# Optimization experiments

Hardware: AMD Instinct MI355X
Metric: run time of the kernel (lower is better)

The kernel has to match this reference:

```python
import jax, jax.numpy as jnp
import numpy as np

B, S, CL = 64, 250, 16
WV, CV, FV, LAB = 50000, 100, 10, 20
WD, CD, CH, FD, HD = 300, 300, 50, 5, 200
T = LAB + 2          # CRF lattice size (labels + START + STOP)
START, STOP = LAB, LAB + 1
H = HD // 2          # hidden per LSTM direction
IN = CH + WD + FD    # 355


def _lstm_dir(x, m, w_ih, w_hh, b):
    # x: [B,S,IN], m: [B,S] bool -> masked unidirectional LSTM (PyTorch gate order i,f,g,o)
    Bn = x.shape[0]
    def step(carry, inp):
        h, c = carry
        xt, mt = inp
        g = xt @ w_ih.T + h @ w_hh.T + b
        i, f, gg, o = jnp.split(g, 4, axis=-1)
        c_new = jax.nn.sigmoid(f) * c + jax.nn.sigmoid(i) * jnp.tanh(gg)
        h_new = jax.nn.sigmoid(o) * jnp.tanh(c_new)
        mt = mt[:, None]
        h = jnp.where(mt, h_new, h)
        c = jnp.where(mt, c_new, c)
        return (h, c), h
    init = (jnp.zeros((Bn, H), x.dtype), jnp.zeros((Bn, H), x.dtype))
    _, hs = jax.lax.scan(step, init, (x.transpose(1, 0, 2), m.T))
    return hs.transpose(1, 0, 2)  # [B,S,H]


def _viterbi(feats, mask, trans):
    # feats: [B,S,T], mask: [B,S] bool, trans: [T,T] (trans[i,j] = score i->j)
    Bn = feats.shape[0]
    delta0 = trans[START][None, :] + feats[:, 0]  # [B,T]
    ident = jnp.arange(T)[None, :]
    def step(delta, inp):
        f_t, m_t = inp                              # [B,T], [B]
        sc = delta[:, :, None] + trans[None]        # [B,T(prev),T(cur)]
        vmax = sc.max(axis=1)
        bp = sc.argmax(axis=1)                      # [B,T]
        m = m_t[:, None]
        delta = jnp.where(m, vmax + f_t, delta)
        bp = jnp.where(m, bp, ident)                # pads: pass-through pointer
        return delta, bp
    delta, bps = jax.lax.scan(step, delta0,
                              (feats[:, 1:].transpose(1, 0, 2), mask[:, 1:].T))
    final = delta + trans[:, STOP][None, :]
    score = final.max(axis=1)                       # [B]
    last = final.argmax(axis=1)                     # [B]
    ar = jnp.arange(Bn)
    def back(tag, bp):
        prev = bp[ar, tag]
        return prev, prev
    _, prevs = jax.lax.scan(back, last, bps, reverse=True)  # [S-1,B]
    tag_seq = jnp.concatenate([prevs.transpose(1, 0), last[:, None]], axis=1)  # [B,S]
    return score, tag_seq


def setup_inputs() -> dict:
    key = jax.random.key(0)
    ks = jax.random.split(key, 20)
    lens = jax.random.randint(ks[0], (B,), S // 2, S + 1)
    mask = (jnp.arange(S)[None, :] < lens[:, None])
    def u(k, shape, scale):
        return jax.random.uniform(k, shape, jnp.float32, -scale, scale)
    return {
        "batch_word": jax.random.randint(ks[1], (B, S), 0, WV),
        "batch_features": jax.random.randint(ks[2], (B, S), 0, FV),
        "batch_wordlen": lens,
        "batch_char": jax.random.randint(ks[3], (B * S, CL), 0, CV),
        "batch_charlen": jax.random.randint(ks[4], (B * S,), 1, CL + 1),
        "batch_charrecover": jnp.arange(B * S),
        "mask": mask,
        "char_emb": u(ks[5], (CV, CD), np.sqrt(3.0 / CD)),
        "word_emb": u(ks[6], (WV, WD), np.sqrt(3.0 / WD)),
        "feat_emb": u(ks[7], (FV, FD), np.sqrt(3.0 / FD)),
        "conv_w": 0.1 * jax.random.normal(ks[8], (CH, CD, 3), jnp.float32),
        "conv_b": jnp.zeros((CH,), jnp.float32),
        "w_ih_f": 0.1 * jax.random.normal(ks[9], (4 * H, IN), jnp.float32),
        "w_hh_f": 0.1 * jax.random.normal(ks[10], (4 * H, H), jnp.float32),
        "b_f": jnp.zeros((4 * H,), jnp.float32),
        "w_ih_b": 0.1 * jax.random.normal(ks[11], (4 * H, IN), jnp.float32),
        "w_hh_b": 0.1 * jax.random.normal(ks[12], (4 * H, H), jnp.float32),
        "b_b": jnp.zeros((4 * H,), jnp.float32),
        "proj_w": 0.1 * jax.random.normal(ks[13], (HD, T), jnp.float32),
        "proj_b": jnp.zeros((T,), jnp.float32),
        "trans": 0.1 * jax.random.normal(ks[14], (T, T), jnp.float32),
    }


def reference(batch_word, batch_features, batch_wordlen, batch_char, batch_charlen,
              batch_charrecover, mask, char_emb, word_emb, feat_emb, conv_w, conv_b,
              w_ih_f, w_hh_f, b_f, w_ih_b, w_hh_b, b_b, proj_w, proj_b, trans):
    # char CNN: embed -> conv1d(k=3, pad=1) -> global max-pool (dropout: eval mode, identity)
    ce = char_emb[batch_char]                          # [B*S, CL, CD]
    conv = jax.lax.conv_general_dilated(
        ce.transpose(0, 2, 1), conv_w, window_strides=(1,), padding=[(1, 1)],
        dimension_numbers=('NCH', 'OIH', 'NCH')) + conv_b[None, :, None]
    char_feat = conv.max(axis=2)                       # [B*S, CH]
    char_feat = char_feat[batch_charrecover].reshape(B, S, CH)
    word_rep = jnp.concatenate(
        [word_emb[batch_word], char_feat, feat_emb[batch_features]], axis=2)  # [B,S,IN]
    # masked BiLSTM (equivalent to pack_padded_sequence: pads never update state)
    h_f = _lstm_dir(word_rep, mask, w_ih_f, w_hh_f, b_f)
    h_b = _lstm_dir(word_rep[:, ::-1], mask[:, ::-1], w_ih_b, w_hh_b, b_b)[:, ::-1]
    lstm_out = jnp.concatenate([h_f, h_b], axis=2)     # [B,S,HD]
    feats = lstm_out @ proj_w + proj_b                 # [B,S,T]
    score, tag_seq = _viterbi(feats, mask, trans)
    return tag_seq
```

## Files before the change

### kernel.cpp

```cpp
#include <hip/hip_runtime.h>
#include <hip/hip_bf16.h>
#include <math.h>

#define WS_U        0
#define WS_WPAD     15360
#define WS_WREP     359424
#define WS_PRE      6503424
#define WS_LSTM     359424
#define WS_FEATS    3559424

__global__ __launch_bounds__(256) void prepw_kernel(
    const float* __restrict__ wf, const float* __restrict__ wb,
    float* __restrict__ w_pad) {
  int idx = blockIdx.x * 256 + threadIdx.x;
  if (idx >= 896 * 384) return;
  int col = idx % 384, row = idx / 384;
  float v = 0.f;
  if (col < 355) {
    if (row < 400)      v = wf[row * 355 + col];
    else if (row < 800) v = wb[(row - 400) * 355 + col];
  }
  w_pad[idx] = v;
}

__global__ __launch_bounds__(256) void u_kernel(
    const float* __restrict__ char_emb, const float* __restrict__ conv_w,
    float* __restrict__ U) {
  int idx = blockIdx.x * 256 + threadIdx.x;
  if (idx >= 15000) return;
  int c = idx / 150, rem = idx % 150, k = rem / 50, o = rem % 50;
  float acc = 0.f;
  for (int i = 0; i < 300; i++)
    acc += char_emb[c * 300 + i] * conv_w[(o * 300 + i) * 3 + k];
  U[idx] = acc;
}

__global__ __launch_bounds__(64) void assemble_kernel(
    const int* __restrict__ batch_word, const int* __restrict__ batch_feats,
    const int* __restrict__ batch_char, const int* __restrict__ recover,
    const float* __restrict__ word_emb, const float* __restrict__ feat_emb,
    const float* __restrict__ conv_b, const float* __restrict__ U,
    float* __restrict__ wrep) {
  int n = blockIdx.x;
  int tid = threadIdx.x;
  __shared__ int ch[16];
  if (tid < 16) ch[tid] = batch_char[(size_t)recover[n] * 16 + tid];
  __syncthreads();
  float* dst = wrep + (size_t)n * 384;
  int w = batch_word[n];
  for (int i = tid; i < 300; i += 64) dst[i] = word_emb[(size_t)w * 300 + i];
  if (tid < 34) {
    int i = 350 + tid;
    dst[i] = (i < 355) ? feat_emb[batch_feats[n] * 5 + (i - 350)] : 0.f;
  }
  if (tid < 50) {
    int o = tid;
    float bo = conv_b[o];
    float m = -1e30f;
#pragma unroll
    for (int l = 0; l < 16; l++) {
      float v = bo + U[(ch[l] * 3 + 1) * 50 + o];
      if (l > 0)  v += U[(ch[l - 1] * 3 + 0) * 50 + o];
      if (l < 15) v += U[(ch[l + 1] * 3 + 2) * 50 + o];
      m = fmaxf(m, v);
    }
    dst[300 + o] = m;
  }
}

__global__ __launch_bounds__(256, 4) void gemm_kernel(
    const float* __restrict__ A, const float* __restrict__ B,
    float* __restrict__ C, const float* __restrict__ bf,
    const float* __restrict__ bb) {
  __shared__ float As[16][128];
  __shared__ float Bs[16][128];
  int tid = threadIdx.x;
  int m0 = blockIdx.x * 128;
  int n0 = blockIdx.y * 128;
  int tx = tid & 15, ty = tid >> 4;
  int lr = tid >> 2;
  int lc = (tid & 3) * 4;
  float acc[8][8];
#pragma unroll
  for (int i = 0; i < 8; i++)
#pragma unroll
    for (int j = 0; j < 8; j++) acc[i][j] = 0.f;

  for (int k0 = 0; k0 < 384; k0 += 16) {
#pragma unroll
    for (int h = 0; h < 2; h++) {
      int row = lr + h * 64;
      float4 av = *(const float4*)(A + (size_t)(m0 + row) * 384 + k0 + lc);
      As[lc + 0][row] = av.x; As[lc + 1][row] = av.y;
      As[lc + 2][row] = av.z; As[lc + 3][row] = av.w;
      float4 bv = *(const float4*)(B + (size_t)(n0 + row) * 384 + k0 + lc);
      Bs[lc + 0][row] = bv.x; Bs[lc + 1][row] = bv.y;
      Bs[lc + 2][row] = bv.z; Bs[lc + 3][row] = bv.w;
    }
    __syncthreads();
#pragma unroll
    for (int k = 0; k < 16; k++) {
      float a[8], b[8];
      *(float4*)&a[0] = *(const float4*)&As[k][ty * 8];
      *(float4*)&a[4] = *(const float4*)&As[k][ty * 8 + 4];
      *(float4*)&b[0] = *(const float4*)&Bs[k][tx * 8];
      *(float4*)&b[4] = *(const float4*)&Bs[k][tx * 8 + 4];
#pragma unroll
      for (int i = 0; i < 8; i++)
#pragma unroll
        for (int j = 0; j < 8; j++) acc[i][j] += a[i] * b[j];
    }
    __syncthreads();
  }
#pragma unroll
  for (int i = 0; i < 8; i++) {
    int m = m0 + ty * 8 + i;
#pragma unroll
    for (int jj = 0; jj < 8; jj++) {
      int j = n0 + tx * 8 + jj;
      if (j < 800) {
        float bias = (j < 400) ? bf[j] : bb[j - 400];
        C[(size_t)m * 800 + j] = acc[i][jj] + bias;
      }
    }
  }
}

__global__ __launch_bounds__(448, 2) void lstm_kernel(
    const float* __restrict__ pre, const float* __restrict__ w_hh_f,
    const float* __restrict__ w_hh_b, const int* __restrict__ wordlen,
    float* __restrict__ lstm_out) {
  int t = threadIdx.x;
  int lane = t & 63;
  int dir = blockIdx.x >> 6;
  int r = blockIdx.x & 63;
  int len = wordlen[r];
  const float* __restrict__ Wh = dir ? w_hh_b : w_hh_f;
  __shared__ __align__(16) float h0[112];
  __shared__ __align__(16) float h1[112];

  const int v = t >> 2;
  const int s = t & 3;
  const bool act = (v < 100);
  const int row = act ? (s * 100 + v) : 0;

  const float4* wr = (const float4*)(Wh + (size_t)row * 100);
  float4 W00 = wr[0],  W01 = wr[1],  W02 = wr[2],  W03 = wr[3],  W04 = wr[4];
  float4 W05 = wr[5],  W06 = wr[6],  W07 = wr[7],  W08 = wr[8],  W09 = wr[9];
  float4 W10 = wr[10], W11 = wr[11], W12 = wr[12], W13 = wr[13], W14 = wr[14];
  float4 W15 = wr[15], W16 = wr[16], W17 = wr[17], W18 = wr[18], W19 = wr[19];
  float4 W20 = wr[20], W21 = wr[21], W22 = wr[22], W23 = wr[23], W24 = wr[24];

  if (t < 112) { h0[t] = 0.f; h1[t] = 0.f; }

  float c_reg = 0.f, h_reg = 0.f;
  const float* __restrict__ pr = pre + dir * 400;
  const int p0 = dir ? 249 : 0;
  const int dp = dir ? -1 : 1;
  const size_t rowbase = (size_t)r * 250;

  float pvA = 0.f, pvB = 0.f;
  if (act) {
    pvA = pr[(rowbase + (size_t)p0) * 800 + row];
    pvB = pr[(rowbase + (size_t)(p0 + dp)) * 800 + row];
  }
  const int cl = (lane < 25) ? lane : 0;
  __syncthreads();

#define RL(x, q) __uint_as_float(__builtin_amdgcn_readlane(__float_as_uint(x), (q)))
#define DOTQ(q, Wq)                                                            \
  g += RL(hch.x, q) * Wq.x + RL(hch.y, q) * Wq.y + RL(hch.z, q) * Wq.z +       \
       RL(hch.w, q) * Wq.w;

#define LSTM_STEP(I, HRD, HWR, PV)                                             \
  do {                                                                         \
    const int p = p0 + dp * (I);                                               \
    const bool valid = (p < len);                           \
    float g = 0.f;                                                             \
    if (valid) {                                                               \
      float4 hch = *(const float4*)&(HRD)[4 * cl];                             \
      g = PV;                                                                  \
      DOTQ(0, W00)  DOTQ(1, W01)  DOTQ(2, W02)  DOTQ(3, W03)  DOTQ(4, W04)    \
      DOTQ(5, W05)  DOTQ(6, W06)  DOTQ(7, W07)  DOTQ(8, W08)  DOTQ(9, W09)    \
      DOTQ(10, W10) DOTQ(11, W11) DOTQ(12, W12) DOTQ(13, W13) DOTQ(14, W14)   \
      DOTQ(15, W15) DOTQ(16, W16) DOTQ(17, W17) DOTQ(18, W18) DOTQ(19, W19)   \
      DOTQ(20, W20) DOTQ(21, W21) DOTQ(22, W22) DOTQ(23, W23) DOTQ(24, W24)   \
    }                                                                          \
    if (act) {                  \
      const int ip = ((I) + 2 < 250) ? (I) + 2 : (I);                          \
      PV = pr[(rowbase + (size_t)(p0 + dp * ip)) * 800 + row];                 \
    }                                                                          \
    if (valid) {                                                               \
      const float gf_in = __shfl_xor(g, 1, 64);       \
      const float gg_in = __shfl_xor(g, 2, 64);       \
      const float go_in = __shfl_xor(g, 3, 64);       \
      if (act && s == 0) {                                                     \
        const float si = 1.f / (1.f + expf(-g));                               \
        const float sf = 1.f / (1.f + expf(-gf_in));                           \
        const float so = 1.f / (1.f + expf(-go_in));                           \
        c_reg = sf * c_reg + si * tanhf(gg_in);                                \
        h_reg = so * tanhf(c_reg);                                             \
        (HWR)[v] = h_reg;                                                      \
        lstm_out[(rowbase + (size_t)p) * 200 + dir * 100 + v] = h_reg;         \
      }                                                                        \
    } else if (act && s == 0) {                                                \
        \
      lstm_out[(rowbase + (size_t)p) * 200 + dir * 100 + v] = h_reg;           \
    }                                                                          \
    __syncthreads();                   \
  } while (0)

#pragma unroll 1
  for (int ii = 0; ii < 250; ii += 2) {
    LSTM_STEP(ii,     h0, h1, pvA);
    LSTM_STEP(ii + 1, h1, h0, pvB);
  }
#undef LSTM_STEP
#undef DOTQ
#undef RL
}

__global__ __launch_bounds__(256) void proj_kernel(
    const float* __restrict__ lstm_out, const float* __restrict__ proj_w,
    const float* __restrict__ proj_b, float* __restrict__ feats) {
  __shared__ float L[8][200];
  int tid = threadIdx.x;
  size_t base = (size_t)blockIdx.x * 8 * 200;
  for (int idx = tid; idx < 1600; idx += 256)
    L[idx / 200][idx % 200] = lstm_out[base + idx];
  __syncthreads();
  int ty = tid >> 5, c = tid & 31;
  if (c < 22) {
    float acc = proj_b[c];
#pragma unroll 8
    for (int k = 0; k < 200; k++) acc += L[ty][k] * proj_w[k * 22 + c];
    feats[((size_t)blockIdx.x * 8 + ty) * 22 + c] = acc;
  }
}

__global__ __launch_bounds__(64) void viterbi_kernel(
    const float* __restrict__ feats, const float* __restrict__ trans,
    const int* __restrict__ wordlen, int* __restrict__ out) {
  int r = blockIdx.x;
  int lane = threadIdx.x;
  __shared__ float dsh[22];
  __shared__ float tsh[22][23];
  __shared__ unsigned char bps[250][22];
  int len = wordlen[r];
  const float* __restrict__ fr = feats + (size_t)r * 250 * 22;
  for (int idx = lane; idx < 484; idx += 64)
    tsh[idx / 22][idx % 22] = trans[idx];
  if (lane < 22) dsh[lane] = trans[20 * 22 + lane] + fr[lane];
  __syncthreads();
  for (int t = 1; t < 250; t++) {
    float best = -1e30f, fv = 0.f;
    int arg = 0;
    if (lane < 22) {
      fv = fr[t * 22 + lane];
#pragma unroll
      for (int k = 0; k < 22; k++) {
        float cand = dsh[k] + tsh[k][lane];
        if (cand > best) { best = cand; arg = k; }
      }
    }
    __syncthreads();
    if (lane < 22) {
      bool valid = t < len;
      if (valid) dsh[lane] = best + fv;
      bps[t][lane] = valid ? (unsigned char)arg : (unsigned char)lane;
    }
    __syncthreads();
  }
  if (lane == 0) {
    float best = -1e30f;
    int last = 0;
#pragma unroll
    for (int k = 0; k < 22; k++) {
      float cand = dsh[k] + tsh[k][21];
      if (cand > best) { best = cand; last = k; }
    }
    int tag = last;
    out[r * 250 + 249] = tag;
    for (int t = 249; t >= 1; t--) {
      tag = bps[t][tag];
      out[r * 250 + t - 1] = tag;
    }
  }
}

extern "C" void kernel_launch(void* const* d_in, const int* in_sizes, int n_in,
                              void* d_out, int out_size, void* d_ws, size_t ws_size,
                              hipStream_t stream) {
  const int* batch_word  = (const int*)d_in[0];
  const int* batch_feats = (const int*)d_in[1];
  const int* wordlen     = (const int*)d_in[2];
  const int* batch_char  = (const int*)d_in[3];
  const int* recover     = (const int*)d_in[5];
  const float* char_emb  = (const float*)d_in[7];
  const float* word_emb  = (const float*)d_in[8];
  const float* feat_emb  = (const float*)d_in[9];
  const float* conv_w    = (const float*)d_in[10];
  const float* conv_b    = (const float*)d_in[11];
  const float* w_ih_f    = (const float*)d_in[12];
  const float* w_hh_f    = (const float*)d_in[13];
  const float* b_f       = (const float*)d_in[14];
  const float* w_ih_b    = (const float*)d_in[15];
  const float* w_hh_b    = (const float*)d_in[16];
  const float* b_b       = (const float*)d_in[17];
  const float* proj_w    = (const float*)d_in[18];
  const float* proj_b    = (const float*)d_in[19];
  const float* trans     = (const float*)d_in[20];
  int* out = (int*)d_out;
  float* ws = (float*)d_ws;

  float* U        = ws + WS_U;
  float* w_pad    = ws + WS_WPAD;
  float* wrep     = ws + WS_WREP;
  float* pre      = ws + WS_PRE;
  float* lstm_out = ws + WS_LSTM;
  float* feats    = ws + WS_FEATS;

  prepw_kernel<<<1344, 256, 0, stream>>>(w_ih_f, w_ih_b, w_pad);
  u_kernel<<<59, 256, 0, stream>>>(char_emb, conv_w, U);
  assemble_kernel<<<16000, 64, 0, stream>>>(batch_word, batch_feats, batch_char,
                                            recover, word_emb, feat_emb, conv_b,
                                            U, wrep);
  dim3 ggrid(125, 7);
  gemm_kernel<<<ggrid, 256, 0, stream>>>(wrep, w_pad, pre, b_f, b_b);
  lstm_kernel<<<128, 448, 0, stream>>>(pre, w_hh_f, w_hh_b, wordlen, lstm_out);
  proj_kernel<<<2000, 256, 0, stream>>>(lstm_out, proj_w, proj_b, feats);
  viterbi_kernel<<<64, 64, 0, stream>>>(feats, trans, wordlen, out);
}
```

Baseline: 862.4 us.

## Split LSTM recurrent dot product across two wave groups with shared-memory reduction

```diff
diff --git a/kernel.cpp b/kernel.cpp
--- a/kernel.cpp
+++ b/kernel.cpp
@@ -126,30 +126,41 @@
   }
 }
 
-__global__ __launch_bounds__(448, 2) void lstm_kernel(
+__global__ __launch_bounds__(896)
+__attribute__((amdgpu_waves_per_eu(3, 4))) void lstm_kernel(
     const float* __restrict__ pre, const float* __restrict__ w_hh_f,
     const float* __restrict__ w_hh_b, const int* __restrict__ wordlen,
     float* __restrict__ lstm_out) {
   int t = threadIdx.x;
   int lane = t & 63;
+  int w = t >> 6;
+  int grp = (w >= 7) ? 1 : 0;
+  int u = (w - grp * 7) * 64 + lane;
   int dir = blockIdx.x >> 6;
   int r = blockIdx.x & 63;
   int len = wordlen[r];
   const float* __restrict__ Wh = dir ? w_hh_b : w_hh_f;
   __shared__ __align__(16) float h0[112];
   __shared__ __align__(16) float h1[112];
-
-  const int v = t >> 2;
-  const int s = t & 3;
+  __shared__ float g_sh[400];
+
+  const int v = u >> 2;
+  const int s = u & 3;
   const bool act = (v < 100);
   const int row = act ? (s * 100 + v) : 0;
-
-  const float4* wr = (const float4*)(Wh + (size_t)row * 100);
-  float4 W00 = wr[0],  W01 = wr[1],  W02 = wr[2],  W03 = wr[3],  W04 = wr[4];
-  float4 W05 = wr[5],  W06 = wr[6],  W07 = wr[7],  W08 = wr[8],  W09 = wr[9];
-  float4 W10 = wr[10], W11 = wr[11], W12 = wr[12], W13 = wr[13], W14 = wr[14];
-  float4 W15 = wr[15], W16 = wr[16], W17 = wr[17], W18 = wr[18], W19 = wr[19];
-  float4 W20 = wr[20], W21 = wr[21], W22 = wr[22], W23 = wr[23], W24 = wr[24];
+  const bool g0act = (grp == 0) && act;
+
+  const float4* wrp = (const float4*)(Wh + (size_t)row * 100) + (grp ? 13 : 0);
+  float4 W00 = wrp[0],  W01 = wrp[1],  W02 = wrp[2],  W03 = wrp[3];
+  float4 W04 = wrp[4],  W05 = wrp[5],  W06 = wrp[6],  W07 = wrp[7];
+  float4 W08 = wrp[8],  W09 = wrp[9],  W10 = wrp[10], W11 = wrp[11];
+  float4 W12 = grp ? make_float4(0.f, 0.f, 0.f, 0.f) : wrp[12];
+
+#define PIN4(W) asm volatile("" : "+v"(W.x), "+v"(W.y), "+v"(W.z), "+v"(W.w))
+  PIN4(W00); PIN4(W01); PIN4(W02); PIN4(W03); PIN4(W04); PIN4(W05);
+  PIN4(W06); PIN4(W07); PIN4(W08); PIN4(W09); PIN4(W10); PIN4(W11);
+  PIN4(W12);
+#undef PIN4
 
   if (t < 112) { h0[t] = 0.f; h1[t] = 0.f; }
 
@@ -159,11 +170,8 @@
   const int dp = dir ? -1 : 1;
   const size_t rowbase = (size_t)r * 250;
 
-  float pvA = 0.f, pvB = 0.f;
-  if (act) {
-    pvA = pr[(rowbase + (size_t)p0) * 800 + row];
-    pvB = pr[(rowbase + (size_t)(p0 + dp)) * 800 + row];
-  }
+  float pv = 0.f;
+  if (g0act) pv = pr[(rowbase + (size_t)p0) * 800 + row];
   const int cl = (lane < 25) ? lane : 0;
   __syncthreads();
 
@@ -172,48 +180,60 @@
   g += RL(hch.x, q) * Wq.x + RL(hch.y, q) * Wq.y + RL(hch.z, q) * Wq.z +       \
        RL(hch.w, q) * Wq.w;
 
-#define LSTM_STEP(I, HRD, HWR, PV)                                             \
+#define LSTM_STEP(I, HRD, HWR)                                                 \
   do {                                                                         \
     const int p = p0 + dp * (I);                                               \
     const bool valid = (p < len);                           \
+    float pvN = 0.f;                                                           \
+    if (g0act) {                \
+      const int ip = ((I) + 1 < 250) ? (I) + 1 : (I);                          \
+      pvN = pr[(rowbase + (size_t)(p0 + dp * ip)) * 800 + row];                \
+    }                                                                          \
     float g = 0.f;                                                             \
     if (valid) {                                                               \
       float4 hch = *(const float4*)&(HRD)[4 * cl];                             \
-      g = PV;                                                                  \
-      DOTQ(0, W00)  DOTQ(1, W01)  DOTQ(2, W02)  DOTQ(3, W03)  DOTQ(4, W04)    \
-      DOTQ(5, W05)  DOTQ(6, W06)  DOTQ(7, W07)  DOTQ(8, W08)  DOTQ(9, W09)    \
-      DOTQ(10, W10) DOTQ(11, W11) DOTQ(12, W12) DOTQ(13, W13) DOTQ(14, W14)   \
-      DOTQ(15, W15) DOTQ(16, W16) DOTQ(17, W17) DOTQ(18, W18) DOTQ(19, W19)   \
-      DOTQ(20, W20) DOTQ(21, W21) DOTQ(22, W22) DOTQ(23, W23) DOTQ(24, W24)   \
+      if (grp == 0) {                                                          \
+        g = pv;                                                                \
+        DOTQ(0, W00)  DOTQ(1, W01)  DOTQ(2, W02)  DOTQ(3, W03)                 \
+        DOTQ(4, W04)  DOTQ(5, W05)  DOTQ(6, W06)  DOTQ(7, W07)                 \
+        DOTQ(8, W08)  DOTQ(9, W09)  DOTQ(10, W10) DOTQ(11, W11)                \
+        DOTQ(12, W12)                                                          \
+      } else {                                                                 \
+        DOTQ(13, W00) DOTQ(14, W01) DOTQ(15, W02) DOTQ(16, W03)                \
+        DOTQ(17, W04) DOTQ(18, W05) DOTQ(19, W06) DOTQ(20, W07)                \
+        DOTQ(21, W08) DOTQ(22, W09) DOTQ(23, W10) DOTQ(24, W11)                \
+        if (act) g_sh[row] = g;                                                \
+      }                                                                        \
     }                                                                          \
-    if (act) {                  \
-      const int ip = ((I) + 2 < 250) ? (I) + 2 : (I);                          \
-      PV = pr[(rowbase + (size_t)(p0 + dp * ip)) * 800 + row];                 \
-    }                                                                          \
+    pv = pvN;                                                                  \
+    __syncthreads();      \
     if (valid) {                                                               \
-      const float gf_in = __shfl_xor(g, 1, 64);       \
-      const float gg_in = __shfl_xor(g, 2, 64);       \
-      const float go_in = __shfl_xor(g, 3, 64);       \
-      if (act && s == 0) {                                                     \
-        const float si = 1.f / (1.f + expf(-g));                               \
-        const float sf = 1.f / (1.f + expf(-gf_in));                           \
-        const float so = 1.f / (1.f + expf(-go_in));                           \
-        c_reg = sf * c_reg + si * tanhf(gg_in);                                \
-        h_reg = so * tanhf(c_reg);                                             \
-        (HWR)[v] = h_reg;                                                      \
-        lstm_out[(rowbase + (size_t)p) * 200 + dir * 100 + v] = h_reg;         \
+      if (grp == 0) {                                                          \
+        const float gfull = g + g_sh[row];                                     \
+        const float gf_in = __shfl_xor(gfull, 1, 64);              \
+        const float gg_in = __shfl_xor(gfull, 2, 64);              \
+        const float go_in = __shfl_xor(gfull, 3, 64);              \
+        if (act && s == 0) {                                                   \
+          const float si = 1.f / (1.f + expf(-gfull));                         \
+          const float sf = 1.f / (1.f + expf(-gf_in));                         \
+          const float so = 1.f / (1.f + expf(-go_in));                         \
+          c_reg = sf * c_reg + si * tanhf(gg_in);                              \
+          h_reg = so * tanhf(c_reg);                                           \
+          (HWR)[v] = h_reg;                                                    \
+          lstm_out[(rowbase + (size_t)p) * 200 + dir * 100 + v] = h_reg;       \
+        }                                                                      \
       }                                                                        \
-    } else if (act && s == 0) {                                                \
-        \
+    } else if (g0act && s == 0) {                                              \
+                                  \
       lstm_out[(rowbase + (size_t)p) * 200 + dir * 100 + v] = h_reg;           \
     }                                                                          \
-    __syncthreads();                   \
+    __syncthreads();                  \
   } while (0)
 
 #pragma unroll 1
   for (int ii = 0; ii < 250; ii += 2) {
-    LSTM_STEP(ii,     h0, h1, pvA);
-    LSTM_STEP(ii + 1, h1, h0, pvB);
+    LSTM_STEP(ii,     h0, h1);
+    LSTM_STEP(ii + 1, h1, h0);
   }
 #undef LSTM_STEP
 #undef DOTQ
@@ -327,7 +347,7 @@
                                             U, wrep);
   dim3 ggrid(125, 7);
   gemm_kernel<<<ggrid, 256, 0, stream>>>(wrep, w_pad, pre, b_f, b_b);
-  lstm_kernel<<<128, 448, 0, stream>>>(pre, w_hh_f, w_hh_b, wordlen, lstm_out);
+  lstm_kernel<<<128, 896, 0, stream>>>(pre, w_hh_f, w_hh_b, wordlen, lstm_out);
   proj_kernel<<<2000, 256, 0, stream>>>(lstm_out, proj_w, proj_b, feats);
   viterbi_kernel<<<64, 64, 0, stream>>>(feats, trans, wordlen, out);
 }
```

Result: faster. 839.4 us (-2.7%).
